# Kernel optimization log

Measured on AMD Instinct MI355X. Metric: run time of the kernel, lower is better.

Reference implementation:

```python
import jax, jax.numpy as jnp
import numpy as np

B, T, H, D = 16, 128, 512, 256
VIN, VOUT = 32000, 32000


def _lstm_cell(xt, h, c, W, U, b):
    # Keras LSTMCell gate order: i, f, g(candidate), o
    z = xt @ W + h @ U + b  # [B, 4H]
    i, f, g, o = jnp.split(z, 4, axis=-1)
    c = jax.nn.sigmoid(f) * c + jax.nn.sigmoid(i) * jnp.tanh(g)
    h = jax.nn.sigmoid(o) * jnp.tanh(c)
    return h, c


def _lstm_seq(x, W, U, b, h0, c0):
    # x: [B,T,Din] -> seq [B,T,H], final (h,c)
    def step(carry, xt):
        h, c = _lstm_cell(xt, carry[0], carry[1], W, U, b)
        return (h, c), h
    (hT, cT), seq = jax.lax.scan(step, (h0, c0), jnp.swapaxes(x, 0, 1))
    return jnp.swapaxes(seq, 0, 1), hT, cT


def setup_inputs() -> dict:
    key = jax.random.key(0)
    ks = jax.random.split(key, 16)
    s = lambda fan: 1.0 / np.sqrt(fan).astype(np.float32)
    f32 = jnp.float32
    return {
        "tokens": jax.random.randint(ks[0], (B, T), 0, VIN + 1),
        "emb": jax.random.normal(ks[1], (VIN + 1, D), f32) * 0.02,
        "W1": jax.random.normal(ks[2], (D, 4 * H), f32) * s(D),
        "U1": jax.random.normal(ks[3], (H, 4 * H), f32) * s(H),
        "b1": jnp.zeros((4 * H,), f32),
        "W2": jax.random.normal(ks[4], (H, 4 * H), f32) * s(H),
        "U2": jax.random.normal(ks[5], (H, 4 * H), f32) * s(H),
        "b2": jnp.zeros((4 * H,), f32),
        "Wd1": jax.random.normal(ks[6], (H, 4 * H), f32) * s(H),
        "Ud1": jax.random.normal(ks[7], (H, 4 * H), f32) * s(H),
        "bd1": jnp.zeros((4 * H,), f32),
        "Wd2": jax.random.normal(ks[8], (H, 4 * H), f32) * s(H),
        "Ud2": jax.random.normal(ks[9], (H, 4 * H), f32) * s(H),
        "bd2": jnp.zeros((4 * H,), f32),
        "Wo": jax.random.normal(ks[10], (2 * H, VOUT + 1), f32) * s(2 * H),
        "bo": jnp.zeros((VOUT + 1,), f32),
    }


def reference(tokens, emb, W1, U1, b1, W2, U2, b2, Wd1, Ud1, bd1, Wd2, Ud2, bd2, Wo, bo):
    x = emb[tokens]  # [B,T,D]
    zeros = jnp.zeros((tokens.shape[0], H), x.dtype)
    seq1, h1, c1 = _lstm_seq(x, W1, U1, b1, zeros, zeros)
    # layer-2 encoder initialized with layer-1 final states (as in source)
    seq2, h2, c2 = _lstm_seq(seq1, W2, U2, b2, h1, c1)

    def dec_step(carry, xt):
        (hA, cA), (hB, cB) = carry
        hA, cA = _lstm_cell(xt, hA, cA, Wd1, Ud1, bd1)
        hB, cB = _lstm_cell(hA, hB, cB, Wd2, Ud2, bd2)
        # global Luong dot attention over full encoder-2 sequence
        score = jax.nn.softmax(jnp.einsum('bsh,bh->bs', seq2, hB), axis=-1)
        ctx = jnp.einsum('bsh,bs->bh', seq2, score)
        out = jnp.concatenate([hB, ctx], axis=-1)  # [B, 2H]
        return ((hA, cA), (hB, cB)), out

    # decoder input is the encoder-2 sequence, time-major
    _, outs = jax.lax.scan(dec_step, ((h1, c1), (h2, c2)), jnp.swapaxes(seq2, 0, 1))
    dec = jnp.swapaxes(outs, 0, 1)  # [B,T,2H]
    logits = dec @ Wo + bo  # [B,T,VOUT+1]
    return jax.nn.softmax(logits, axis=-1)
```

## Files before the change

### kernel.cpp

```cpp
#include <hip/hip_runtime.h>
#include <hip/hip_bf16.h>
#include <math.h>

#define Bq   16
#define Tq   128
#define Hq   512
#define Dq   256
#define G4H  2048
#define MR   2048
#define VO   32001
#define NPAD 32128
#define NBLK 32
#define BH   (Bq * Hq)
#define SENTW 0x7FC0u
#define SENT64 0x7FC07FC07FC07FC0ull

typedef unsigned int u32;
typedef unsigned long long u64;
typedef __attribute__((ext_vector_type(4))) float f32x4;
typedef __attribute__((ext_vector_type(8))) short bfrag;
typedef __attribute__((ext_vector_type(4))) float facc;

__device__ __forceinline__ float bf2f(short s) {
  union { unsigned u; float f; } v; v.u = ((unsigned)(unsigned short)s) << 16; return v.f;
}
__device__ __forceinline__ short f2bf(float f) {
  union { float f; unsigned u; } v; v.f = f;
  unsigned r = (v.u + 0x7fffu + ((v.u >> 16) & 1u)) >> 16;
  return (short)r;
}
__device__ __forceinline__ float asf(u32 u) {
  union { u32 u; float f; } v; v.u = u; return v.f;
}
__device__ __forceinline__ float sigm(float x) { return 1.0f / (1.0f + expf(-x)); }

__device__ __forceinline__ void ic_store64(u64* p, u64 v) {
  __hip_atomic_store(p, v, __ATOMIC_RELAXED, __HIP_MEMORY_SCOPE_AGENT);
}
__device__ __forceinline__ u64 ic_load64(const u64* p) {
  return __hip_atomic_load(p, __ATOMIC_RELAXED, __HIP_MEMORY_SCOPE_AGENT);
}

__device__ __forceinline__ void* swz(void* plane, int row, int byteoff) {
  return (void*)((char*)plane + row * 1040 + (byteoff ^ ((row & 7) << 4)));
}

__global__ __launch_bounds__(256) void k_fill(u64* __restrict__ p, int n) {
  int i = blockIdx.x * 256 + threadIdx.x;
  if (i < n) p[i] = SENT64;
}

__global__ __launch_bounds__(256) void k_transcvt(const float* __restrict__ in,
                                                  short* __restrict__ out,
                                                  int R, int N, int perm) {
  __shared__ float tile[32][33];
  int nb = blockIdx.x * 32, rb = blockIdx.y * 32;
  int tx = threadIdx.x & 31, ty = threadIdx.x >> 5;
  for (int i = 0; i < 4; ++i) {
    int r = rb + ty + i * 8;
    int n = nb + tx;
    tile[ty + i * 8][tx] = (n < N) ? in[(size_t)r * N + n] : 0.0f;
  }
  __syncthreads();
  for (int i = 0; i < 4; ++i) {
    int n = nb + ty + i * 8;
    int orow = perm ? (((n & 511) << 2) | (n >> 9)) : n;
    out[(size_t)orow * R + rb + tx] = f2bf(tile[tx][ty + i * 8]);
  }
}

__global__ __launch_bounds__(256) void k_gather(const int* __restrict__ tokens,
                                                const float* __restrict__ emb,
                                                short* __restrict__ xbf) {
  int row = blockIdx.x;
  int t = row >> 4, b = row & 15;
  int tok = tokens[b * Tq + t];
  xbf[(size_t)row * Dq + threadIdx.x] = f2bf(emb[(size_t)tok * Dq + threadIdx.x]);
}

__global__ __launch_bounds__(256) void k_gemm(const short* __restrict__ A,
                                              const short* __restrict__ BT,
                                              float* __restrict__ C,
                                              const float* __restrict__ bias,
                                              int M, int Nreal, int K, int ldc,
                                              int permb) {
  __shared__ short lA[128 * 64];
  __shared__ short lB[128 * 64];
  const int tid = threadIdx.x;
  const int wave = tid >> 6, lane = tid & 63;
  const int l15 = lane & 15, l4 = lane >> 4;
  const int m0 = blockIdx.y * 128, n0 = blockIdx.x * 128;
  const int wm = (wave >> 1) * 64, wn = (wave & 1) * 64;
  facc acc[4][4] = {};

  for (int k0 = 0; k0 < K; k0 += 64) {
    __syncthreads();
    for (int i = 0; i < 4; ++i) {
      int c = i * 256 + wave * 64 + lane;
      int r = c >> 3, q = c & 7;
      int qs = q ^ (r & 7);
      const short* ga = A + (size_t)(m0 + r) * K + k0 + qs * 8;
      const short* gb = BT + (size_t)(n0 + r) * K + k0 + qs * 8;
      short* la = lA + (size_t)(i * 256 + wave * 64) * 8;
      short* lb = lB + (size_t)(i * 256 + wave * 64) * 8;
      __builtin_amdgcn_global_load_lds((const __attribute__((address_space(1))) u32*)ga,
                                       (__attribute__((address_space(3))) u32*)la, 16, 0, 0);
      __builtin_amdgcn_global_load_lds((const __attribute__((address_space(1))) u32*)gb,
                                       (__attribute__((address_space(3))) u32*)lb, 16, 0, 0);
    }
    __syncthreads();
    for (int ks = 0; ks < 2; ++ks) {
      bfrag a[4], b[4];
      for (int mi = 0; mi < 4; ++mi) {
        int r = wm + mi * 16 + l15;
        int qs = (ks * 4 + l4) ^ (r & 7);
        a[mi] = *(const bfrag*)&lA[r * 64 + qs * 8];
      }
      for (int ni = 0; ni < 4; ++ni) {
        int r = wn + ni * 16 + l15;
        int qs = (ks * 4 + l4) ^ (r & 7);
        b[ni] = *(const bfrag*)&lB[r * 64 + qs * 8];
      }
      for (int mi = 0; mi < 4; ++mi)
        for (int ni = 0; ni < 4; ++ni)
          acc[mi][ni] = __builtin_amdgcn_mfma_f32_16x16x32_bf16(a[mi], b[ni], acc[mi][ni], 0, 0, 0);
    }
  }
  for (int ni = 0; ni < 4; ++ni) {
    int col = n0 + wn + ni * 16 + l15;
    if (col >= Nreal) continue;
    int bcol = permb ? (((col & 3) << 9) | (col >> 2)) : col;
    float bs = bias ? bias[bcol] : 0.0f;
    for (int mi = 0; mi < 4; ++mi) {
      int rb = m0 + wm + mi * 16 + l4 * 4;
      facc v = acc[mi][ni];
      C[(size_t)(rb + 0) * ldc + col] = v[0] + bs;
      C[(size_t)(rb + 1) * ldc + col] = v[1] + bs;
      C[(size_t)(rb + 2) * ldc + col] = v[2] + bs;
      C[(size_t)(rb + 3) * ldc + col] = v[3] + bs;
    }
  }
}


__global__ __launch_bounds__(512, 1) void k_rec(const float* __restrict__ XW,
                                                const short* __restrict__ UT,
                                                const float* __restrict__ hinit,
                                                const float* __restrict__ cinit,
                                                u64* __restrict__ hbuf,
                                                float* __restrict__ hfin,
                                                float* __restrict__ cfin,
                                                short* __restrict__ seq_bf) {
  __shared__ short lh[2][16][520];
  __shared__ float zt[8][16][20];
  const int tid = threadIdx.x;
  const int wv = tid >> 6, lane = tid & 63;
  const int l15 = lane & 15, l4 = lane >> 4;
  const int kh = wv >> 2;
  const int gw = blockIdx.x * 4 + (wv & 3);
  const int bb = lane >> 2, jj = lane & 3;
  const int hidx = gw * 4 + jj;

  bfrag ur[8];
  {
    const short* ub = UT + (size_t)(gw * 16 + l15) * Hq + kh * 256 + l4 * 8;
    #pragma unroll
    for (int ks = 0; ks < 8; ++ks) ur[ks] = *(const bfrag*)&ub[ks * 32];
  }
  float c = 0.0f;
  if (wv < 4) {
    c = cinit ? cinit[bb * Hq + hidx] : 0.0f;
    float hv = hinit ? hinit[bb * Hq + hidx] : 0.0f;
    int hi_ = (int)(unsigned short)f2bf(hv);
    int lo_ = (int)(unsigned short)f2bf(hv - bf2f((short)hi_));
    int hi2 = __shfl_xor(hi_, 1), lo2 = __shfl_xor(lo_, 1);
    if ((jj & 1) == 0) {
      u64 v = (u64)((u32)hi_ | ((u32)hi2 << 16)) | ((u64)((u32)lo_ | ((u32)lo2 << 16)) << 32);
      ic_store64(&hbuf[(bb * Hq + hidx) >> 1], v);
    }
  }

  for (int s = 0; s < Tq; ++s) {
    f32x4 xg = {};
    if (wv < 4) xg = *(const f32x4*)&XW[(size_t)(s * Bq + bb) * G4H + hidx * 4];
    const u64* hsrc = hbuf + (size_t)s * 4096;
    u64 v[8];
    for (;;) {
      #pragma unroll
      for (int it = 0; it < 8; ++it) v[it] = ic_load64(&hsrc[it * 512 + tid]);
      u32 bad = 0;
      #pragma unroll
      for (int it = 0; it < 8; ++it) bad |= (((u32)v[it] & 0xFFFFu) == SENTW);
      if (!bad) break;
      __builtin_amdgcn_s_sleep(1);
    }
    #pragma unroll
    for (int it = 0; it < 8; ++it) {
      int i = it * 512 + tid;
      int b = i >> 8, bo = (i & 255) * 4;
      *(u32*)swz(&lh[0][0][0], b, bo) = (u32)v[it];
      *(u32*)swz(&lh[1][0][0], b, bo) = (u32)(v[it] >> 32);
    }
    __syncthreads();
    facc a0 = {}, a1 = {};
    #pragma unroll
    for (int ks = 0; ks < 8; ++ks) {
      int bo = kh * 512 + ks * 64 + l4 * 16;
      bfrag ah = *(const bfrag*)swz(&lh[0][0][0], l15, bo);
      bfrag al = *(const bfrag*)swz(&lh[1][0][0], l15, bo);
      a0 = __builtin_amdgcn_mfma_f32_16x16x32_bf16(ah, ur[ks], a0, 0, 0, 0);
      a1 = __builtin_amdgcn_mfma_f32_16x16x32_bf16(al, ur[ks], a1, 0, 0, 0);
    }
    a0 += a1;
    *(f32x4*)&zt[wv][l15][l4 * 4] = a0;
    __syncthreads();
    if (wv < 4) {
      float zi = zt[wv][4 * jj + 0][bb] + zt[wv + 4][4 * jj + 0][bb] + xg[0];
      float zf = zt[wv][4 * jj + 1][bb] + zt[wv + 4][4 * jj + 1][bb] + xg[1];
      float zg = zt[wv][4 * jj + 2][bb] + zt[wv + 4][4 * jj + 2][bb] + xg[2];
      float zo = zt[wv][4 * jj + 3][bb] + zt[wv + 4][4 * jj + 3][bb] + xg[3];
      c = sigm(zf) * c + sigm(zi) * tanhf(zg);
      float hN = sigm(zo) * tanhf(c);
      int hi_ = (int)(unsigned short)f2bf(hN);
      int lo_ = (int)(unsigned short)f2bf(hN - bf2f((short)hi_));
      int hi2 = __shfl_xor(hi_, 1), lo2 = __shfl_xor(lo_, 1);
      if (s < Tq - 1 && (jj & 1) == 0) {
        u64 v2 = (u64)((u32)hi_ | ((u32)hi2 << 16)) | ((u64)((u32)lo_ | ((u32)lo2 << 16)) << 32);
        ic_store64(&hbuf[(size_t)(s + 1) * 4096 + ((bb * Hq + hidx) >> 1)], v2);
      }
      seq_bf[(size_t)(s * Bq + bb) * Hq + hidx] = (short)hi_;
      if (s == Tq - 1) { hfin[bb * Hq + hidx] = hN; cfin[bb * Hq + hidx] = c; }
    }
  }
}

__global__ __launch_bounds__(512, 1) void k_dec2(const float* __restrict__ XW,
                                                 const short* __restrict__ U1T,
                                                 const short* __restrict__ W2T,
                                                 const short* __restrict__ U2T,
                                                 const float* __restrict__ bd2,
                                                 const float* __restrict__ h1f, const float* __restrict__ c1f,
                                                 const float* __restrict__ h2f, const float* __restrict__ c2f,
                                                 u64* __restrict__ hAbuf, u64* __restrict__ hBbuf,
                                                 short* __restrict__ hBseq_bf, short* __restrict__ dec_bf) {
  __shared__ short lA[2][16][520];
  __shared__ short lB[2][16][520];
  __shared__ float ztA[8][16][20];
  __shared__ float ztB[8][16][20];
  const int tid = threadIdx.x;
  const int wv = tid >> 6, lane = tid & 63;
  const int l15 = lane & 15, l4 = lane >> 4;
  const int kh = wv >> 2;
  const int gw = blockIdx.x * 4 + (wv & 3);
  const int bb = lane >> 2, jj = lane & 3;
  const int hidx = gw * 4 + jj;

  bfrag u1r[8], w2r[8], u2r[8];
  {
    size_t ro = (size_t)(gw * 16 + l15) * Hq + kh * 256 + l4 * 8;
    #pragma unroll
    for (int ks = 0; ks < 8; ++ks) {
      u1r[ks] = *(const bfrag*)&U1T[ro + ks * 32];
      w2r[ks] = *(const bfrag*)&W2T[ro + ks * 32];
      u2r[ks] = *(const bfrag*)&U2T[ro + ks * 32];
    }
  }
  float cc = 0.0f, bdi = 0, bdf = 0, bdg = 0, bdo = 0;
  {
    const float* cf = (wv < 4) ? c1f : c2f;
    const float* hf = (wv < 4) ? h1f : h2f;
    cc = cf[bb * Hq + hidx];
    float hv = hf[bb * Hq + hidx];
    int hi_ = (int)(unsigned short)f2bf(hv);
    int lo_ = (int)(unsigned short)f2bf(hv - bf2f((short)hi_));
    int hi2 = __shfl_xor(hi_, 1), lo2 = __shfl_xor(lo_, 1);
    if ((jj & 1) == 0) {
      u64 v = (u64)((u32)hi_ | ((u32)hi2 << 16)) | ((u64)((u32)lo_ | ((u32)lo2 << 16)) << 32);
      int pi = (bb * Hq + hidx) >> 1;
      if (wv < 4) {
        ic_store64(&hAbuf[pi], v);
      } else {
        ic_store64(&hBbuf[pi], v);
        ic_store64(&hBbuf[4096 + pi], v);
      }
    }
    if (wv >= 4) {
      bdi = bd2[hidx]; bdf = bd2[Hq + hidx];
      bdg = bd2[2 * Hq + hidx]; bdo = bd2[3 * Hq + hidx];
    }
  }

  for (int p = 0; p <= Tq; ++p) {
    f32x4 xg = {};
    if (wv < 4 && p < Tq) xg = *(const f32x4*)&XW[(size_t)(p * Bq + bb) * G4H + hidx * 4];
    const u64* asrc = hAbuf + (size_t)p * 4096;
    const u64* bsrc = hBbuf + (size_t)p * 4096;
    u64 va[8], vb[8];
    for (;;) {
      #pragma unroll
      for (int it = 0; it < 8; ++it) {
        va[it] = ic_load64(&asrc[it * 512 + tid]);
        vb[it] = ic_load64(&bsrc[it * 512 + tid]);
      }
      u32 bad = 0;
      #pragma unroll
      for (int it = 0; it < 8; ++it) {
        bad |= (((u32)va[it] & 0xFFFFu) == SENTW);
        bad |= (((u32)vb[it] & 0xFFFFu) == SENTW);
      }
      if (!bad) break;
      __builtin_amdgcn_s_sleep(1);
    }
    #pragma unroll
    for (int it = 0; it < 8; ++it) {
      int i = it * 512 + tid;
      int b = i >> 8, bo = (i & 255) * 4;
      *(u32*)swz(&lA[0][0][0], b, bo) = (u32)va[it];
      *(u32*)swz(&lA[1][0][0], b, bo) = (u32)(va[it] >> 32);
      *(u32*)swz(&lB[0][0][0], b, bo) = (u32)vb[it];
      *(u32*)swz(&lB[1][0][0], b, bo) = (u32)(vb[it] >> 32);
    }
    __syncthreads();

    facc a0 = {}, a1 = {}, b0 = {}, b1 = {}, b2 = {}, b3 = {};
    #pragma unroll
    for (int ks = 0; ks < 8; ++ks) {
      int bo = kh * 512 + ks * 64 + l4 * 16;
      bfrag ah = *(const bfrag*)swz(&lA[0][0][0], l15, bo);
      bfrag al = *(const bfrag*)swz(&lA[1][0][0], l15, bo);
      if (p < Tq) {
        a0 = __builtin_amdgcn_mfma_f32_16x16x32_bf16(ah, u1r[ks], a0, 0, 0, 0);
        a1 = __builtin_amdgcn_mfma_f32_16x16x32_bf16(al, u1r[ks], a1, 0, 0, 0);
      }
      if (p >= 1) {
        bfrag hh = *(const bfrag*)swz(&lB[0][0][0], l15, bo);
        bfrag hl = *(const bfrag*)swz(&lB[1][0][0], l15, bo);
        b0 = __builtin_amdgcn_mfma_f32_16x16x32_bf16(ah, w2r[ks], b0, 0, 0, 0);
        b1 = __builtin_amdgcn_mfma_f32_16x16x32_bf16(al, w2r[ks], b1, 0, 0, 0);
        b2 = __builtin_amdgcn_mfma_f32_16x16x32_bf16(hh, u2r[ks], b2, 0, 0, 0);
        b3 = __builtin_amdgcn_mfma_f32_16x16x32_bf16(hl, u2r[ks], b3, 0, 0, 0);
      }
    }
    if (p < Tq) { a0 += a1; *(f32x4*)&ztA[wv][l15][l4 * 4] = a0; }
    if (p >= 1) { b0 += b1; b0 += b2; b0 += b3; *(f32x4*)&ztB[wv][l15][l4 * 4] = b0; }
    __syncthreads();

    if (wv < 4 && p < Tq) {
      float zi = ztA[wv][4 * jj + 0][bb] + ztA[wv + 4][4 * jj + 0][bb] + xg[0];
      float zf = ztA[wv][4 * jj + 1][bb] + ztA[wv + 4][4 * jj + 1][bb] + xg[1];
      float zg = ztA[wv][4 * jj + 2][bb] + ztA[wv + 4][4 * jj + 2][bb] + xg[2];
      float zo = ztA[wv][4 * jj + 3][bb] + ztA[wv + 4][4 * jj + 3][bb] + xg[3];
      cc = sigm(zf) * cc + sigm(zi) * tanhf(zg);
      float hN = sigm(zo) * tanhf(cc);
      int hi_ = (int)(unsigned short)f2bf(hN);
      int lo_ = (int)(unsigned short)f2bf(hN - bf2f((short)hi_));
      int hi2 = __shfl_xor(hi_, 1), lo2 = __shfl_xor(lo_, 1);
      if ((jj & 1) == 0) {
        u64 v = (u64)((u32)hi_ | ((u32)hi2 << 16)) | ((u64)((u32)lo_ | ((u32)lo2 << 16)) << 32);
        ic_store64(&hAbuf[(size_t)(p + 1) * 4096 + ((bb * Hq + hidx) >> 1)], v);
      }
    }
    if (wv >= 4 && p >= 1) {
      int s = p - 1;
      int pw = wv - 4;
      float zi = ztB[pw][4 * jj + 0][bb] + ztB[wv][4 * jj + 0][bb] + bdi;
      float zf = ztB[pw][4 * jj + 1][bb] + ztB[wv][4 * jj + 1][bb] + bdf;
      float zg = ztB[pw][4 * jj + 2][bb] + ztB[wv][4 * jj + 2][bb] + bdg;
      float zo = ztB[pw][4 * jj + 3][bb] + ztB[wv][4 * jj + 3][bb] + bdo;
      cc = sigm(zf) * cc + sigm(zi) * tanhf(zg);
      float hN = sigm(zo) * tanhf(cc);
      int hi_ = (int)(unsigned short)f2bf(hN);
      int lo_ = (int)(unsigned short)f2bf(hN - bf2f((short)hi_));
      int hi2 = __shfl_xor(hi_, 1), lo2 = __shfl_xor(lo_, 1);
      if (p < Tq && (jj & 1) == 0) {
        u64 v = (u64)((u32)hi_ | ((u32)hi2 << 16)) | ((u64)((u32)lo_ | ((u32)lo2 << 16)) << 32);
        ic_store64(&hBbuf[(size_t)(p + 1) * 4096 + ((bb * Hq + hidx) >> 1)], v);
      }
      hBseq_bf[(size_t)(s * Bq + bb) * Hq + hidx] = (short)hi_;
      dec_bf[((size_t)bb * Tq + s) * (2 * Hq) + hidx] = (short)hi_;
    }
  }
}

__global__ __launch_bounds__(256) void k_attn(const short* __restrict__ seq2b,
                                              const short* __restrict__ hqb,
                                              short* __restrict__ decb) {
  int blk = blockIdx.x;
  int b = blk >> 7, t = blk & 127;
  __shared__ u32 q[256];
  __shared__ float part[256];
  __shared__ float p[Tq];
  int tid = threadIdx.x;
  q[tid] = *(const u32*)&hqb[(size_t)(t * Bq + b) * Hq + tid * 2];
  __syncthreads();
  {
    int s = tid >> 1, half = tid & 1;
    const u32* row = (const u32*)&seq2b[(size_t)(s * Bq + b) * Hq + half * 256];
    const u32* qh = q + half * 128;
    float a = 0.0f;
    #pragma unroll 8
    for (int k = 0; k < 128; ++k) {
      u32 r = row[k], qq = qh[k];
      a += asf(r << 16) * asf(qq << 16) + asf(r & 0xFFFF0000u) * asf(qq & 0xFFFF0000u);
    }
    part[tid] = a;
  }
  __syncthreads();
  if (tid < 64) {
    float v0 = part[2 * tid] + part[2 * tid + 1];
    float v1 = part[2 * (tid + 64)] + part[2 * (tid + 64) + 1];
    float mx = fmaxf(v0, v1);
    for (int off = 32; off; off >>= 1) mx = fmaxf(mx, __shfl_xor(mx, off));
    float e0 = __expf(v0 - mx), e1 = __expf(v1 - mx);
    float sm = e0 + e1;
    for (int off = 32; off; off >>= 1) sm += __shfl_xor(sm, off);
    float inv = 1.0f / sm;
    p[tid] = e0 * inv; p[tid + 64] = e1 * inv;
  }
  __syncthreads();
  float c0 = 0.0f, c1 = 0.0f;
  for (int s = 0; s < Tq; ++s) {
    float ps = p[s];
    u32 r = *(const u32*)&seq2b[(size_t)(s * Bq + b) * Hq + tid * 2];
    c0 += ps * asf(r << 16);
    c1 += ps * asf(r & 0xFFFF0000u);
  }
  u32 o = ((u32)(unsigned short)f2bf(c0)) | (((u32)(unsigned short)f2bf(c1)) << 16);
  *(u32*)&decb[(size_t)(b * Tq + t) * (2 * Hq) + Hq + tid * 2] = o;
}

__global__ __launch_bounds__(256) void k_softmax(float* __restrict__ L) {
  int row = blockIdx.x;
  float* p = L + (size_t)row * VO;
  int tid = threadIdx.x;
  float m = -3.0e38f, s = 0.0f;
  for (int i = tid; i < VO; i += 256) {
    float v = p[i];
    float mn = fmaxf(m, v);
    s = s * __expf(m - mn) + __expf(v - mn);
    m = mn;
  }
  __shared__ float sm[256], ss[256];
  sm[tid] = m; ss[tid] = s;
  __syncthreads();
  for (int off = 128; off; off >>= 1) {
    if (tid < off) {
      float m2 = sm[tid + off], s2 = ss[tid + off];
      float mn = fmaxf(sm[tid], m2);
      ss[tid] = ss[tid] * __expf(sm[tid] - mn) + s2 * __expf(m2 - mn);
      sm[tid] = mn;
    }
    __syncthreads();
  }
  float M = sm[0], IS = 1.0f / ss[0];
  for (int i = tid; i < VO; i += 256) {
    p[i] = __expf(p[i] - M) * IS;
  }
}

extern "C" void kernel_launch(void* const* d_in, const int* in_sizes, int n_in,
                              void* d_out, int out_size, void* d_ws, size_t ws_size,
                              hipStream_t stream) {
  const int*   tokens = (const int*)d_in[0];
  const float* emb    = (const float*)d_in[1];
  const float* W1     = (const float*)d_in[2];
  const float* U1     = (const float*)d_in[3];
  const float* b1     = (const float*)d_in[4];
  const float* W2     = (const float*)d_in[5];
  const float* U2     = (const float*)d_in[6];
  const float* b2     = (const float*)d_in[7];
  const float* Wd1    = (const float*)d_in[8];
  const float* Ud1    = (const float*)d_in[9];
  const float* bd1    = (const float*)d_in[10];
  const float* Wd2    = (const float*)d_in[11];
  const float* Ud2    = (const float*)d_in[12];
  const float* bd2    = (const float*)d_in[13];
  const float* Wo     = (const float*)d_in[14];
  const float* bo     = (const float*)d_in[15];
  float* out = (float*)d_out;

  size_t off = 0;
  char* base = (char*)d_ws;
  auto alloc = [&](size_t bytes) -> void* {
    void* p = base + off;
    off += (bytes + 255) & ~(size_t)255;
    return p;
  };
  short* x_bf    = (short*)alloc((size_t)MR * Dq * 2);
  short* W1T     = (short*)alloc((size_t)G4H * Dq * 2);
  short* W2T     = (short*)alloc((size_t)G4H * Hq * 2);
  short* Wd1T    = (short*)alloc((size_t)G4H * Hq * 2);
  short* WoT     = (short*)alloc((size_t)NPAD * (2 * Hq) * 2);
  short* U1T     = (short*)alloc((size_t)G4H * Hq * 2);
  short* U2T     = (short*)alloc((size_t)G4H * Hq * 2);
  short* Ud1T    = (short*)alloc((size_t)G4H * Hq * 2);
  short* Ud2T    = (short*)alloc((size_t)G4H * Hq * 2);
  short* Wd2T    = (short*)alloc((size_t)G4H * Hq * 2);
  float* XW      = (float*)alloc((size_t)MR * G4H * 4);
  short* seq1_bf = (short*)alloc((size_t)MR * Hq * 2);
  short* seq2_bf = (short*)alloc((size_t)MR * Hq * 2);
  short* hBseqbf = (short*)alloc((size_t)MR * Hq * 2);
  short* dec_bf  = (short*)alloc((size_t)MR * 2 * Hq * 2);
  u64*   hflow   = (u64*)alloc((size_t)514 * 4096 * 8);
  u64*   h1buf   = hflow;
  u64*   h2buf   = hflow + (size_t)128 * 4096;
  u64*   hAbuf   = hflow + (size_t)256 * 4096;
  u64*   hBbuf   = hflow + (size_t)385 * 4096;
  float* h1f = (float*)alloc(BH * 4);
  float* c1f = (float*)alloc(BH * 4);
  float* h2f = (float*)alloc(BH * 4);
  float* c2f = (float*)alloc(BH * 4);
  (void)ws_size; (void)in_sizes; (void)n_in; (void)out_size;

  {
    int n = 514 * 4096;
    k_fill<<<(n + 255) / 256, 256, 0, stream>>>(hflow, n);
  }

  k_transcvt<<<dim3(G4H / 32, Dq / 32), 256, 0, stream>>>(W1, W1T, Dq, G4H, 1);
  k_transcvt<<<dim3(G4H / 32, Hq / 32), 256, 0, stream>>>(W2, W2T, Hq, G4H, 1);
  k_transcvt<<<dim3(G4H / 32, Hq / 32), 256, 0, stream>>>(Wd1, Wd1T, Hq, G4H, 1);
  k_transcvt<<<dim3(G4H / 32, Hq / 32), 256, 0, stream>>>(U1, U1T, Hq, G4H, 1);
  k_transcvt<<<dim3(G4H / 32, Hq / 32), 256, 0, stream>>>(U2, U2T, Hq, G4H, 1);
  k_transcvt<<<dim3(G4H / 32, Hq / 32), 256, 0, stream>>>(Ud1, Ud1T, Hq, G4H, 1);
  k_transcvt<<<dim3(G4H / 32, Hq / 32), 256, 0, stream>>>(Ud2, Ud2T, Hq, G4H, 1);
  k_transcvt<<<dim3(G4H / 32, Hq / 32), 256, 0, stream>>>(Wd2, Wd2T, Hq, G4H, 1);
  k_transcvt<<<dim3(NPAD / 32, (2 * Hq) / 32), 256, 0, stream>>>(Wo, WoT, 2 * Hq, VO, 0);

  k_gather<<<MR, 256, 0, stream>>>(tokens, emb, x_bf);

  k_gemm<<<dim3(G4H / 128, MR / 128), 256, 0, stream>>>(x_bf, W1T, XW, b1, MR, G4H, Dq, G4H, 1);
  k_rec<<<NBLK, 512, 0, stream>>>(XW, U1T, nullptr, nullptr, h1buf, h1f, c1f, seq1_bf);

  k_gemm<<<dim3(G4H / 128, MR / 128), 256, 0, stream>>>(seq1_bf, W2T, XW, b2, MR, G4H, Hq, G4H, 1);
  k_rec<<<NBLK, 512, 0, stream>>>(XW, U2T, h1f, c1f, h2buf, h2f, c2f, seq2_bf);

  k_gemm<<<dim3(G4H / 128, MR / 128), 256, 0, stream>>>(seq2_bf, Wd1T, XW, bd1, MR, G4H, Hq, G4H, 1);
  k_dec2<<<NBLK, 512, 0, stream>>>(XW, Ud1T, Wd2T, Ud2T, bd2, h1f, c1f, h2f, c2f,
                                   hAbuf, hBbuf, hBseqbf, dec_bf);

  k_attn<<<MR, 256, 0, stream>>>(seq2_bf, hBseqbf, dec_bf);
  k_gemm<<<dim3(NPAD / 128, MR / 128), 256, 0, stream>>>(dec_bf, WoT, out, bo, MR, VO, 2 * Hq, VO, 0);
  k_softmax<<<MR, 256, 0, stream>>>(out);
}
```

Before: 2.311 ms.

## Merge the recurrent LSTM layers into one persistent multi-group mega-kernel

Replaces the separate encoder and decoder recurrence kernels, and the input-projection GEMMs between them, with a single 128-block persistent kernel. The blocks form four 32-block groups, one per LSTM layer. Each downstream layer computes its input projection per timestep inside the recurrence, from a bf16 stream published by the upstream layer. Final h/c states are handed between groups through NaN-sentinel flags, so the decoder's first layer can run alongside encoder layer 2. This removes two GEMM launches and kernel boundaries. In exchange it needs all 128 blocks co-resident, adds more MFMAs per step, and relies on bounded spin-waits.

After: 2.500 ms. +8.2%, slower.

```diff
diff --git a/kernel.cpp b/kernel.cpp
--- a/kernel.cpp
+++ b/kernel.cpp
@@ -10,10 +10,11 @@
 #define MR   2048
 #define VO   32001
 #define NPAD 32128
-#define NBLK 32
 #define BH   (Bq * Hq)
 #define SENTW 0x7FC0u
 #define SENT64 0x7FC07FC07FC07FC0ull
+#define NANW 0x7FC00000u
+#define SPINCAP (1 << 20)
 
 typedef unsigned int u32;
 typedef unsigned long long u64;
@@ -32,6 +33,9 @@
 __device__ __forceinline__ float asf(u32 u) {
   union { u32 u; float f; } v; v.u = u; return v.f;
 }
+__device__ __forceinline__ u32 fbits(float f) {
+  union { float f; u32 u; } v; v.f = f; return v.u;
+}
 __device__ __forceinline__ float sigm(float x) { return 1.0f / (1.0f + expf(-x)); }
 
 __device__ __forceinline__ void ic_store64(u64* p, u64 v) {
@@ -40,14 +44,42 @@
 __device__ __forceinline__ u64 ic_load64(const u64* p) {
   return __hip_atomic_load(p, __ATOMIC_RELAXED, __HIP_MEMORY_SCOPE_AGENT);
 }
+__device__ __forceinline__ void ic_store32(u32* p, u32 v) {
+  __hip_atomic_store(p, v, __ATOMIC_RELAXED, __HIP_MEMORY_SCOPE_AGENT);
+}
+__device__ __forceinline__ u32 ic_load32(const u32* p) {
+  return __hip_atomic_load(p, __ATOMIC_RELAXED, __HIP_MEMORY_SCOPE_AGENT);
+}
 
 __device__ __forceinline__ void* swz(void* plane, int row, int byteoff) {
   return (void*)((char*)plane + row * 1040 + (byteoff ^ ((row & 7) << 4)));
+}
+
+__device__ __forceinline__ void stage_h(void* p0, void* p1, const u64 v[8]) {
+  #pragma unroll
+  for (int it = 0; it < 8; ++it) {
+    int i = it * 512 + threadIdx.x;
+    int b = i >> 8, bo = (i & 255) * 4;
+    *(u32*)swz(p0, b, bo) = (u32)v[it];
+    *(u32*)swz(p1, b, bo) = (u32)(v[it] >> 32);
+  }
+}
+__device__ __forceinline__ void stage_x(void* p0, const u32 w[8]) {
+  #pragma unroll
+  for (int it = 0; it < 8; ++it) {
+    int i = it * 512 + threadIdx.x;
+    int b = i >> 8, bo = (i & 255) * 4;
+    *(u32*)swz(p0, b, bo) = w[it];
+  }
 }
 
 __global__ __launch_bounds__(256) void k_fill(u64* __restrict__ p, int n) {
   int i = blockIdx.x * 256 + threadIdx.x;
   if (i < n) p[i] = SENT64;
+}
+__global__ __launch_bounds__(256) void k_fillf(u32* __restrict__ p, int n) {
+  int i = blockIdx.x * 256 + threadIdx.x;
+  if (i < n) p[i] = NANW;
 }
 
 __global__ __launch_bounds__(256) void k_transcvt(const float* __restrict__ in,
@@ -142,242 +174,186 @@
   }
 }
 
-
-__global__ __launch_bounds__(512, 1) void k_rec(const float* __restrict__ XW,
-                                                const short* __restrict__ UT,
-                                                const float* __restrict__ hinit,
-                                                const float* __restrict__ cinit,
-                                                u64* __restrict__ hbuf,
-                                                float* __restrict__ hfin,
-                                                float* __restrict__ cfin,
-                                                short* __restrict__ seq_bf) {
-  __shared__ short lh[2][16][520];
+__global__ __launch_bounds__(512, 1) void k_mega(
+    const float* __restrict__ XW,
+    const short* __restrict__ U1T, const short* __restrict__ U2T,
+    const short* __restrict__ W2T, const short* __restrict__ Ud1T,
+    const short* __restrict__ Wd1T, const short* __restrict__ Ud2T,
+    const short* __restrict__ Wd2T,
+    const float* __restrict__ b2, const float* __restrict__ bd1,
+    const float* __restrict__ bd2,
+    u64* __restrict__ h1buf, u64* __restrict__ h2buf,
+    u64* __restrict__ hAbuf, u64* __restrict__ hBbuf,
+    u32* __restrict__ xs1, u32* __restrict__ xs2,
+    u32* __restrict__ h1f, u32* __restrict__ c1f,
+    u32* __restrict__ h2f, u32* __restrict__ c2f,
+    short* __restrict__ seq2_bf, short* __restrict__ hBseq_bf,
+    short* __restrict__ dec_bf)
+{
+  __shared__ short pl[4][16][520];
   __shared__ float zt[8][16][20];
+  const int grp  = blockIdx.x >> 5;
+  const int rank = blockIdx.x & 31;
   const int tid = threadIdx.x;
   const int wv = tid >> 6, lane = tid & 63;
   const int l15 = lane & 15, l4 = lane >> 4;
   const int kh = wv >> 2;
-  const int gw = blockIdx.x * 4 + (wv & 3);
+  const int gw = rank * 4 + (wv & 3);
   const int bb = lane >> 2, jj = lane & 3;
   const int hidx = gw * 4 + jj;
-
-  bfrag ur[8];
+  const int idx = bb * Hq + hidx;
+  const int pi = idx >> 1;
+
+  const short* urs = (grp == 0) ? U1T : (grp == 1) ? U2T : (grp == 2) ? Ud1T : Ud2T;
+  const short* wrs = (grp == 1) ? W2T : (grp == 2) ? Wd1T : (grp == 3) ? Wd2T : U1T;
+  const float* bias = (grp == 1) ? b2 : (grp == 2) ? bd1 : bd2;
+  u64* own = (grp == 0) ? h1buf : (grp == 1) ? h2buf : (grp == 2) ? hAbuf : hBbuf;
+  const u32* xin = (grp == 1) ? xs1 : xs2;
+  u32* xout = (grp == 0) ? xs1 : (grp == 1) ? xs2 : nullptr;
+
+  bfrag ur[8], wr[8];
   {
-    const short* ub = UT + (size_t)(gw * 16 + l15) * Hq + kh * 256 + l4 * 8;
+    size_t ro = (size_t)(gw * 16 + l15) * Hq + kh * 256 + l4 * 8;
     #pragma unroll
-    for (int ks = 0; ks < 8; ++ks) ur[ks] = *(const bfrag*)&ub[ks * 32];
+    for (int ks = 0; ks < 8; ++ks) {
+      ur[ks] = *(const bfrag*)&urs[ro + ks * 32];
+      wr[ks] = *(const bfrag*)&wrs[ro + ks * 32];
+    }
+  }
+  float bi = 0, bf_ = 0, bg_ = 0, bo_ = 0;
+  if (grp != 0 && wv < 4) {
+    bi = bias[hidx]; bf_ = bias[Hq + hidx];
+    bg_ = bias[2 * Hq + hidx]; bo_ = bias[3 * Hq + hidx];
   }
   float c = 0.0f;
   if (wv < 4) {
-    c = cinit ? cinit[bb * Hq + hidx] : 0.0f;
-    float hv = hinit ? hinit[bb * Hq + hidx] : 0.0f;
+    float hv = 0.0f;
+    if (grp != 0) {
+      const u32* hf = (grp == 3) ? h2f : h1f;
+      const u32* cf = (grp == 3) ? c2f : c1f;
+      u32 hw = NANW, cw = NANW;
+      for (int spin = 0; spin < SPINCAP; ++spin) {
+        hw = ic_load32(&hf[idx]); cw = ic_load32(&cf[idx]);
+        if (hw != NANW && cw != NANW) break;
+        __builtin_amdgcn_s_sleep(16);
+      }
+      hv = asf(hw); c = asf(cw);
+    }
     int hi_ = (int)(unsigned short)f2bf(hv);
     int lo_ = (int)(unsigned short)f2bf(hv - bf2f((short)hi_));
     int hi2 = __shfl_xor(hi_, 1), lo2 = __shfl_xor(lo_, 1);
     if ((jj & 1) == 0) {
       u64 v = (u64)((u32)hi_ | ((u32)hi2 << 16)) | ((u64)((u32)lo_ | ((u32)lo2 << 16)) << 32);
-      ic_store64(&hbuf[(bb * Hq + hidx) >> 1], v);
+      ic_store64(&own[pi], v);
     }
   }
 
   for (int s = 0; s < Tq; ++s) {
     f32x4 xg = {};
-    if (wv < 4) xg = *(const f32x4*)&XW[(size_t)(s * Bq + bb) * G4H + hidx * 4];
-    const u64* hsrc = hbuf + (size_t)s * 4096;
-    u64 v[8];
-    for (;;) {
-      #pragma unroll
-      for (int it = 0; it < 8; ++it) v[it] = ic_load64(&hsrc[it * 512 + tid]);
-      u32 bad = 0;
-      #pragma unroll
-      for (int it = 0; it < 8; ++it) bad |= (((u32)v[it] & 0xFFFFu) == SENTW);
-      if (!bad) break;
-      __builtin_amdgcn_s_sleep(1);
-    }
-    #pragma unroll
-    for (int it = 0; it < 8; ++it) {
-      int i = it * 512 + tid;
-      int b = i >> 8, bo = (i & 255) * 4;
-      *(u32*)swz(&lh[0][0][0], b, bo) = (u32)v[it];
-      *(u32*)swz(&lh[1][0][0], b, bo) = (u32)(v[it] >> 32);
-    }
+    if (grp == 0 && wv < 4)
+      xg = *(const f32x4*)&XW[(size_t)(s * Bq + bb) * G4H + hidx * 4];
+
+    u64 v[8], vx[8];
+    u32 w[8];
+    const u64* ph = own + (size_t)s * 4096 + tid;
+    if (grp == 0) {
+      for (int spin = 0;; ++spin) {
+        #pragma unroll
+        for (int it = 0; it < 8; ++it) v[it] = ic_load64(&ph[it * 512]);
+        u32 bad = 0;
+        #pragma unroll
+        for (int it = 0; it < 8; ++it) bad |= (((u32)v[it] & 0xFFFFu) == SENTW);
+        if (!bad || spin >= SPINCAP) break;
+        __builtin_amdgcn_s_sleep(1);
+      }
+    } else if (grp != 3) {
+      const u32* px = xin + (size_t)s * 4096 + tid;
+      for (int spin = 0;; ++spin) {
+        #pragma unroll
+        for (int it = 0; it < 8; ++it) v[it] = ic_load64(&ph[it * 512]);
+        #pragma unroll
+        for (int it = 0; it < 8; ++it) w[it] = ic_load32(&px[it * 512]);
+        u32 bad = 0;
+        #pragma unroll
+        for (int it = 0; it < 8; ++it) {
+          bad |= (((u32)v[it] & 0xFFFFu) == SENTW);
+          bad |= ((w[it] & 0xFFFFu) == SENTW);
+        }
+        if (!bad || spin >= SPINCAP) break;
+        __builtin_amdgcn_s_sleep(1);
+      }
+    } else {
+      const u64* pa = hAbuf + (size_t)(s + 1) * 4096 + tid;
+      for (int spin = 0;; ++spin) {
+        #pragma unroll
+        for (int it = 0; it < 8; ++it) v[it]  = ic_load64(&ph[it * 512]);
+        #pragma unroll
+        for (int it = 0; it < 8; ++it) vx[it] = ic_load64(&pa[it * 512]);
+        u32 bad = 0;
+        #pragma unroll
+        for (int it = 0; it < 8; ++it) {
+          bad |= (((u32)v[it]  & 0xFFFFu) == SENTW);
+          bad |= (((u32)vx[it] & 0xFFFFu) == SENTW);
+        }
+        if (!bad || spin >= SPINCAP) break;
+        __builtin_amdgcn_s_sleep(1);
+      }
+    }
+    stage_h(&pl[0][0][0], &pl[1][0][0], v);
+    if (grp == 1 || grp == 2) stage_x(&pl[2][0][0], w);
+    else if (grp == 3)        stage_h(&pl[2][0][0], &pl[3][0][0], vx);
     __syncthreads();
-    facc a0 = {}, a1 = {};
+
+    facc a0 = {}, a1 = {}, a2 = {}, a3 = {};
     #pragma unroll
     for (int ks = 0; ks < 8; ++ks) {
       int bo = kh * 512 + ks * 64 + l4 * 16;
-      bfrag ah = *(const bfrag*)swz(&lh[0][0][0], l15, bo);
-      bfrag al = *(const bfrag*)swz(&lh[1][0][0], l15, bo);
-      a0 = __builtin_amdgcn_mfma_f32_16x16x32_bf16(ah, ur[ks], a0, 0, 0, 0);
-      a1 = __builtin_amdgcn_mfma_f32_16x16x32_bf16(al, ur[ks], a1, 0, 0, 0);
+      bfrag hh = *(const bfrag*)swz(&pl[0][0][0], l15, bo);
+      bfrag hl = *(const bfrag*)swz(&pl[1][0][0], l15, bo);
+      a0 = __builtin_amdgcn_mfma_f32_16x16x32_bf16(hh, ur[ks], a0, 0, 0, 0);
+      a1 = __builtin_amdgcn_mfma_f32_16x16x32_bf16(hl, ur[ks], a1, 0, 0, 0);
+      if (grp == 1 || grp == 2) {
+        bfrag xh = *(const bfrag*)swz(&pl[2][0][0], l15, bo);
+        a2 = __builtin_amdgcn_mfma_f32_16x16x32_bf16(xh, wr[ks], a2, 0, 0, 0);
+      } else if (grp == 3) {
+        bfrag xh = *(const bfrag*)swz(&pl[2][0][0], l15, bo);
+        bfrag xl = *(const bfrag*)swz(&pl[3][0][0], l15, bo);
+        a2 = __builtin_amdgcn_mfma_f32_16x16x32_bf16(xh, wr[ks], a2, 0, 0, 0);
+        a3 = __builtin_amdgcn_mfma_f32_16x16x32_bf16(xl, wr[ks], a3, 0, 0, 0);
+      }
     }
     a0 += a1;
+    if (grp != 0) a0 += a2;
+    if (grp == 3) a0 += a3;
     *(f32x4*)&zt[wv][l15][l4 * 4] = a0;
     __syncthreads();
+
     if (wv < 4) {
-      float zi = zt[wv][4 * jj + 0][bb] + zt[wv + 4][4 * jj + 0][bb] + xg[0];
-      float zf = zt[wv][4 * jj + 1][bb] + zt[wv + 4][4 * jj + 1][bb] + xg[1];
-      float zg = zt[wv][4 * jj + 2][bb] + zt[wv + 4][4 * jj + 2][bb] + xg[2];
-      float zo = zt[wv][4 * jj + 3][bb] + zt[wv + 4][4 * jj + 3][bb] + xg[3];
+      float zi = zt[wv][4 * jj + 0][bb] + zt[wv + 4][4 * jj + 0][bb];
+      float zf = zt[wv][4 * jj + 1][bb] + zt[wv + 4][4 * jj + 1][bb];
+      float zg = zt[wv][4 * jj + 2][bb] + zt[wv + 4][4 * jj + 2][bb];
+      float zo = zt[wv][4 * jj + 3][bb] + zt[wv + 4][4 * jj + 3][bb];
+      if (grp == 0) { zi += xg[0]; zf += xg[1]; zg += xg[2]; zo += xg[3]; }
+      else          { zi += bi;    zf += bf_;   zg += bg_;   zo += bo_;  }
       c = sigm(zf) * c + sigm(zi) * tanhf(zg);
       float hN = sigm(zo) * tanhf(c);
       int hi_ = (int)(unsigned short)f2bf(hN);
       int lo_ = (int)(unsigned short)f2bf(hN - bf2f((short)hi_));
       int hi2 = __shfl_xor(hi_, 1), lo2 = __shfl_xor(lo_, 1);
-      if (s < Tq - 1 && (jj & 1) == 0) {
-        u64 v2 = (u64)((u32)hi_ | ((u32)hi2 << 16)) | ((u64)((u32)lo_ | ((u32)lo2 << 16)) << 32);
-        ic_store64(&hbuf[(size_t)(s + 1) * 4096 + ((bb * Hq + hidx) >> 1)], v2);
-      }
-      seq_bf[(size_t)(s * Bq + bb) * Hq + hidx] = (short)hi_;
-      if (s == Tq - 1) { hfin[bb * Hq + hidx] = hN; cfin[bb * Hq + hidx] = c; }
-    }
-  }
-}
-
-__global__ __launch_bounds__(512, 1) void k_dec2(const float* __restrict__ XW,
-                                                 const short* __restrict__ U1T,
-                                                 const short* __restrict__ W2T,
-                                                 const short* __restrict__ U2T,
-                                                 const float* __restrict__ bd2,
-                                                 const float* __restrict__ h1f, const float* __restrict__ c1f,
-                                                 const float* __restrict__ h2f, const float* __restrict__ c2f,
-                                                 u64* __restrict__ hAbuf, u64* __restrict__ hBbuf,
-                                                 short* __restrict__ hBseq_bf, short* __restrict__ dec_bf) {
-  __shared__ short lA[2][16][520];
-  __shared__ short lB[2][16][520];
-  __shared__ float ztA[8][16][20];
-  __shared__ float ztB[8][16][20];
-  const int tid = threadIdx.x;
-  const int wv = tid >> 6, lane = tid & 63;
-  const int l15 = lane & 15, l4 = lane >> 4;
-  const int kh = wv >> 2;
-  const int gw = blockIdx.x * 4 + (wv & 3);
-  const int bb = lane >> 2, jj = lane & 3;
-  const int hidx = gw * 4 + jj;
-
-  bfrag u1r[8], w2r[8], u2r[8];
-  {
-    size_t ro = (size_t)(gw * 16 + l15) * Hq + kh * 256 + l4 * 8;
-    #pragma unroll
-    for (int ks = 0; ks < 8; ++ks) {
-      u1r[ks] = *(const bfrag*)&U1T[ro + ks * 32];
-      w2r[ks] = *(const bfrag*)&W2T[ro + ks * 32];
-      u2r[ks] = *(const bfrag*)&U2T[ro + ks * 32];
-    }
-  }
-  float cc = 0.0f, bdi = 0, bdf = 0, bdg = 0, bdo = 0;
-  {
-    const float* cf = (wv < 4) ? c1f : c2f;
-    const float* hf = (wv < 4) ? h1f : h2f;
-    cc = cf[bb * Hq + hidx];
-    float hv = hf[bb * Hq + hidx];
-    int hi_ = (int)(unsigned short)f2bf(hv);
-    int lo_ = (int)(unsigned short)f2bf(hv - bf2f((short)hi_));
-    int hi2 = __shfl_xor(hi_, 1), lo2 = __shfl_xor(lo_, 1);
-    if ((jj & 1) == 0) {
-      u64 v = (u64)((u32)hi_ | ((u32)hi2 << 16)) | ((u64)((u32)lo_ | ((u32)lo2 << 16)) << 32);
-      int pi = (bb * Hq + hidx) >> 1;
-      if (wv < 4) {
-        ic_store64(&hAbuf[pi], v);
-      } else {
-        ic_store64(&hBbuf[pi], v);
-        ic_store64(&hBbuf[4096 + pi], v);
-      }
-    }
-    if (wv >= 4) {
-      bdi = bd2[hidx]; bdf = bd2[Hq + hidx];
-      bdg = bd2[2 * Hq + hidx]; bdo = bd2[3 * Hq + hidx];
-    }
-  }
-
-  for (int p = 0; p <= Tq; ++p) {
-    f32x4 xg = {};
-    if (wv < 4 && p < Tq) xg = *(const f32x4*)&XW[(size_t)(p * Bq + bb) * G4H + hidx * 4];
-    const u64* asrc = hAbuf + (size_t)p * 4096;
-    const u64* bsrc = hBbuf + (size_t)p * 4096;
-    u64 va[8], vb[8];
-    for (;;) {
-      #pragma unroll
-      for (int it = 0; it < 8; ++it) {
-        va[it] = ic_load64(&asrc[it * 512 + tid]);
-        vb[it] = ic_load64(&bsrc[it * 512 + tid]);
-      }
-      u32 bad = 0;
-      #pragma unroll
-      for (int it = 0; it < 8; ++it) {
-        bad |= (((u32)va[it] & 0xFFFFu) == SENTW);
-        bad |= (((u32)vb[it] & 0xFFFFu) == SENTW);
-      }
-      if (!bad) break;
-      __builtin_amdgcn_s_sleep(1);
-    }
-    #pragma unroll
-    for (int it = 0; it < 8; ++it) {
-      int i = it * 512 + tid;
-      int b = i >> 8, bo = (i & 255) * 4;
-      *(u32*)swz(&lA[0][0][0], b, bo) = (u32)va[it];
-      *(u32*)swz(&lA[1][0][0], b, bo) = (u32)(va[it] >> 32);
-      *(u32*)swz(&lB[0][0][0], b, bo) = (u32)vb[it];
-      *(u32*)swz(&lB[1][0][0], b, bo) = (u32)(vb[it] >> 32);
-    }
-    __syncthreads();
-
-    facc a0 = {}, a1 = {}, b0 = {}, b1 = {}, b2 = {}, b3 = {};
-    #pragma unroll
-    for (int ks = 0; ks < 8; ++ks) {
-      int bo = kh * 512 + ks * 64 + l4 * 16;
-      bfrag ah = *(const bfrag*)swz(&lA[0][0][0], l15, bo);
-      bfrag al = *(const bfrag*)swz(&lA[1][0][0], l15, bo);
-      if (p < Tq) {
-        a0 = __builtin_amdgcn_mfma_f32_16x16x32_bf16(ah, u1r[ks], a0, 0, 0, 0);
-        a1 = __builtin_amdgcn_mfma_f32_16x16x32_bf16(al, u1r[ks], a1, 0, 0, 0);
-      }
-      if (p >= 1) {
-        bfrag hh = *(const bfrag*)swz(&lB[0][0][0], l15, bo);
-        bfrag hl = *(const bfrag*)swz(&lB[1][0][0], l15, bo);
-        b0 = __builtin_amdgcn_mfma_f32_16x16x32_bf16(ah, w2r[ks], b0, 0, 0, 0);
-        b1 = __builtin_amdgcn_mfma_f32_16x16x32_bf16(al, w2r[ks], b1, 0, 0, 0);
-        b2 = __builtin_amdgcn_mfma_f32_16x16x32_bf16(hh, u2r[ks], b2, 0, 0, 0);
-        b3 = __builtin_amdgcn_mfma_f32_16x16x32_bf16(hl, u2r[ks], b3, 0, 0, 0);
-      }
-    }
-    if (p < Tq) { a0 += a1; *(f32x4*)&ztA[wv][l15][l4 * 4] = a0; }
-    if (p >= 1) { b0 += b1; b0 += b2; b0 += b3; *(f32x4*)&ztB[wv][l15][l4 * 4] = b0; }
-    __syncthreads();
-
-    if (wv < 4 && p < Tq) {
-      float zi = ztA[wv][4 * jj + 0][bb] + ztA[wv + 4][4 * jj + 0][bb] + xg[0];
-      float zf = ztA[wv][4 * jj + 1][bb] + ztA[wv + 4][4 * jj + 1][bb] + xg[1];
-      float zg = ztA[wv][4 * jj + 2][bb] + ztA[wv + 4][4 * jj + 2][bb] + xg[2];
-      float zo = ztA[wv][4 * jj + 3][bb] + ztA[wv + 4][4 * jj + 3][bb] + xg[3];
-      cc = sigm(zf) * cc + sigm(zi) * tanhf(zg);
-      float hN = sigm(zo) * tanhf(cc);
-      int hi_ = (int)(unsigned short)f2bf(hN);
-      int lo_ = (int)(unsigned short)f2bf(hN - bf2f((short)hi_));
-      int hi2 = __shfl_xor(hi_, 1), lo2 = __shfl_xor(lo_, 1);
       if ((jj & 1) == 0) {
-        u64 v = (u64)((u32)hi_ | ((u32)hi2 << 16)) | ((u64)((u32)lo_ | ((u32)lo2 << 16)) << 32);
-        ic_store64(&hAbuf[(size_t)(p + 1) * 4096 + ((bb * Hq + hidx) >> 1)], v);
-      }
-    }
-    if (wv >= 4 && p >= 1) {
-      int s = p - 1;
-      int pw = wv - 4;
-      float zi = ztB[pw][4 * jj + 0][bb] + ztB[wv][4 * jj + 0][bb] + bdi;
-      float zf = ztB[pw][4 * jj + 1][bb] + ztB[wv][4 * jj + 1][bb] + bdf;
-      float zg = ztB[pw][4 * jj + 2][bb] + ztB[wv][4 * jj + 2][bb] + bdg;
-      float zo = ztB[pw][4 * jj + 3][bb] + ztB[wv][4 * jj + 3][bb] + bdo;
-      cc = sigm(zf) * cc + sigm(zi) * tanhf(zg);
-      float hN = sigm(zo) * tanhf(cc);
-      int hi_ = (int)(unsigned short)f2bf(hN);
-      int lo_ = (int)(unsigned short)f2bf(hN - bf2f((short)hi_));
-      int hi2 = __shfl_xor(hi_, 1), lo2 = __shfl_xor(lo_, 1);
-      if (p < Tq && (jj & 1) == 0) {
-        u64 v = (u64)((u32)hi_ | ((u32)hi2 << 16)) | ((u64)((u32)lo_ | ((u32)lo2 << 16)) << 32);
-        ic_store64(&hBbuf[(size_t)(p + 1) * 4096 + ((bb * Hq + hidx) >> 1)], v);
-      }
-      hBseq_bf[(size_t)(s * Bq + bb) * Hq + hidx] = (short)hi_;
-      dec_bf[((size_t)bb * Tq + s) * (2 * Hq) + hidx] = (short)hi_;
+        u64 pv = (u64)((u32)hi_ | ((u32)hi2 << 16)) | ((u64)((u32)lo_ | ((u32)lo2 << 16)) << 32);
+        ic_store64(&own[(size_t)(s + 1) * 4096 + pi], pv);
+        if (xout) ic_store32(&xout[(size_t)s * 4096 + pi], (u32)pv);
+      }
+      if (grp == 1) seq2_bf[(size_t)(s * Bq + bb) * Hq + hidx] = (short)hi_;
+      if (grp == 3) {
+        hBseq_bf[(size_t)(s * Bq + bb) * Hq + hidx] = (short)hi_;
+        dec_bf[((size_t)bb * Tq + s) * (2 * Hq) + hidx] = (short)hi_;
+      }
+      if (s == Tq - 1) {
+        if (grp == 0) { ic_store32(&h1f[idx], fbits(hN)); ic_store32(&c1f[idx], fbits(c)); }
+        if (grp == 1) { ic_store32(&h2f[idx], fbits(hN)); ic_store32(&c2f[idx], fbits(c)); }
+      }
     }
   }
 }
@@ -488,41 +464,43 @@
   };
   short* x_bf    = (short*)alloc((size_t)MR * Dq * 2);
   short* W1T     = (short*)alloc((size_t)G4H * Dq * 2);
-  short* W2T     = (short*)alloc((size_t)G4H * Hq * 2);
-  short* Wd1T    = (short*)alloc((size_t)G4H * Hq * 2);
   short* WoT     = (short*)alloc((size_t)NPAD * (2 * Hq) * 2);
   short* U1T     = (short*)alloc((size_t)G4H * Hq * 2);
   short* U2T     = (short*)alloc((size_t)G4H * Hq * 2);
+  short* W2T     = (short*)alloc((size_t)G4H * Hq * 2);
   short* Ud1T    = (short*)alloc((size_t)G4H * Hq * 2);
+  short* Wd1T    = (short*)alloc((size_t)G4H * Hq * 2);
   short* Ud2T    = (short*)alloc((size_t)G4H * Hq * 2);
   short* Wd2T    = (short*)alloc((size_t)G4H * Hq * 2);
   float* XW      = (float*)alloc((size_t)MR * G4H * 4);
-  short* seq1_bf = (short*)alloc((size_t)MR * Hq * 2);
   short* seq2_bf = (short*)alloc((size_t)MR * Hq * 2);
   short* hBseqbf = (short*)alloc((size_t)MR * Hq * 2);
   short* dec_bf  = (short*)alloc((size_t)MR * 2 * Hq * 2);
-  u64*   hflow   = (u64*)alloc((size_t)514 * 4096 * 8);
-  u64*   h1buf   = hflow;
-  u64*   h2buf   = hflow + (size_t)128 * 4096;
-  u64*   hAbuf   = hflow + (size_t)256 * 4096;
-  u64*   hBbuf   = hflow + (size_t)385 * 4096;
-  float* h1f = (float*)alloc(BH * 4);
-  float* c1f = (float*)alloc(BH * 4);
-  float* h2f = (float*)alloc(BH * 4);
-  float* c2f = (float*)alloc(BH * 4);
+  u64*   hflow   = (u64*)alloc((size_t)516 * 4096 * 8);
+  u32*   xs1     = (u32*)alloc((size_t)128 * 4096 * 4);
+  u32*   xs2     = (u32*)alloc((size_t)128 * 4096 * 4);
+  u32*   h1f     = (u32*)alloc(BH * 4);
+  u32*   c1f     = (u32*)alloc(BH * 4);
+  u32*   h2f     = (u32*)alloc(BH * 4);
+  u32*   c2f     = (u32*)alloc(BH * 4);
+  u64* h1buf = hflow;
+  u64* h2buf = hflow + (size_t)129 * 4096;
+  u64* hAbuf = hflow + (size_t)258 * 4096;
+  u64* hBbuf = hflow + (size_t)387 * 4096;
   (void)ws_size; (void)in_sizes; (void)n_in; (void)out_size;
 
   {
-    int n = 514 * 4096;
-    k_fill<<<(n + 255) / 256, 256, 0, stream>>>(hflow, n);
+    int n64 = 516 * 4096 + 2 * (128 * 4096 / 2);
+    k_fill<<<(n64 + 255) / 256, 256, 0, stream>>>(hflow, n64);
+    k_fillf<<<(4 * BH + 255) / 256, 256, 0, stream>>>(h1f, 4 * BH);
   }
 
   k_transcvt<<<dim3(G4H / 32, Dq / 32), 256, 0, stream>>>(W1, W1T, Dq, G4H, 1);
-  k_transcvt<<<dim3(G4H / 32, Hq / 32), 256, 0, stream>>>(W2, W2T, Hq, G4H, 1);
-  k_transcvt<<<dim3(G4H / 32, Hq / 32), 256, 0, stream>>>(Wd1, Wd1T, Hq, G4H, 1);
   k_transcvt<<<dim3(G4H / 32, Hq / 32), 256, 0, stream>>>(U1, U1T, Hq, G4H, 1);
   k_transcvt<<<dim3(G4H / 32, Hq / 32), 256, 0, stream>>>(U2, U2T, Hq, G4H, 1);
+  k_transcvt<<<dim3(G4H / 32, Hq / 32), 256, 0, stream>>>(W2, W2T, Hq, G4H, 1);
   k_transcvt<<<dim3(G4H / 32, Hq / 32), 256, 0, stream>>>(Ud1, Ud1T, Hq, G4H, 1);
+  k_transcvt<<<dim3(G4H / 32, Hq / 32), 256, 0, stream>>>(Wd1, Wd1T, Hq, G4H, 1);
   k_transcvt<<<dim3(G4H / 32, Hq / 32), 256, 0, stream>>>(Ud2, Ud2T, Hq, G4H, 1);
   k_transcvt<<<dim3(G4H / 32, Hq / 32), 256, 0, stream>>>(Wd2, Wd2T, Hq, G4H, 1);
   k_transcvt<<<dim3(NPAD / 32, (2 * Hq) / 32), 256, 0, stream>>>(Wo, WoT, 2 * Hq, VO, 0);
@@ -530,14 +508,12 @@
   k_gather<<<MR, 256, 0, stream>>>(tokens, emb, x_bf);
 
   k_gemm<<<dim3(G4H / 128, MR / 128), 256, 0, stream>>>(x_bf, W1T, XW, b1, MR, G4H, Dq, G4H, 1);
-  k_rec<<<NBLK, 512, 0, stream>>>(XW, U1T, nullptr, nullptr, h1buf, h1f, c1f, seq1_bf);
-
-  k_gemm<<<dim3(G4H / 128, MR / 128), 256, 0, stream>>>(seq1_bf, W2T, XW, b2, MR, G4H, Hq, G4H, 1);
-  k_rec<<<NBLK, 512, 0, stream>>>(XW, U2T, h1f, c1f, h2buf, h2f, c2f, seq2_bf);
-
-  k_gemm<<<dim3(G4H / 128, MR / 128), 256, 0, stream>>>(seq2_bf, Wd1T, XW, bd1, MR, G4H, Hq, G4H, 1);
-  k_dec2<<<NBLK, 512, 0, stream>>>(XW, Ud1T, Wd2T, Ud2T, bd2, h1f, c1f, h2f, c2f,
-                                   hAbuf, hBbuf, hBseqbf, dec_bf);
+
+  k_mega<<<128, 512, 0, stream>>>(XW, U1T, U2T, W2T, Ud1T, Wd1T, Ud2T, Wd2T,
+                                  b2, bd1, bd2,
+                                  h1buf, h2buf, hAbuf, hBbuf, xs1, xs2,
+                                  h1f, c1f, h2f, c2f,
+                                  seq2_bf, hBseqbf, dec_bf);
 
   k_attn<<<MR, 256, 0, stream>>>(seq2_bf, hBseqbf, dec_bf);
   k_gemm<<<dim3(NPAD / 128, MR / 128), 256, 0, stream>>>(dec_bf, WoT, out, bo, MR, VO, 2 * Hq, VO, 0);
```
